# Kernel optimization log

Hardware: AMD Instinct MI355X
Metric: run time of the kernel (lower is better)

The kernel has to match this reference:

```python
import jax, jax.numpy as jnp
import numpy as np

K = 3
EPS = 1e-5

def diff_conv(x, Tf, Tb, W, b):
    terms = [x]
    xf = x
    for _ in range(K):
        xf = jnp.einsum('mn,bnc->bmc', Tf, xf)
        terms.append(xf)
    xb = x
    for _ in range(K):
        xb = jnp.einsum('mn,bnc->bmc', Tb, xb)
        terms.append(xb)
    z = jnp.concatenate(terms, axis=-1)  # (B,N,(2K+1)*C)
    return z @ W + b

def layer_norm(x, gamma, beta):
    mu = jnp.mean(x, axis=-1, keepdims=True)
    var = jnp.var(x, axis=-1, keepdims=True)
    return (x - mu) * jax.lax.rsqrt(var + EPS) * gamma + beta

def dcgru_cell(x, h, Tf, Tb, Wg, bg, Wc, bc, gamma, beta):
    xh = jnp.concatenate([x, h], axis=-1)
    gates = jax.nn.sigmoid(diff_conv(xh, Tf, Tb, Wg, bg))
    r, u = jnp.split(gates, 2, axis=-1)
    xrh = jnp.concatenate([x, r * h], axis=-1)
    c = jnp.tanh(diff_conv(xrh, Tf, Tb, Wc, bc))
    h_new = (1.0 - u) * h + u * c
    return layer_norm(h_new, gamma, beta)

def setup_inputs() -> dict:
    key = jax.random.key(0)
    B, T, N, F, H = 32, 8, 512, 16, 128
    ks = jax.random.split(key, 16)
    s = 0.02
    n_terms = 2 * K + 1
    d0 = (F + H) * n_terms   # layer 0 combined diffusion dim
    d1 = (H + H) * n_terms   # layer 1
    inp = {
        'x_seq': jax.random.normal(ks[0], (B, T, N, F), dtype=jnp.float32),
        'T_f': jax.random.uniform(ks[1], (N, N), dtype=jnp.float32) / N,
        'T_b': jax.random.uniform(ks[2], (N, N), dtype=jnp.float32) / N,
        'Wg0': jax.random.normal(ks[3], (d0, 2 * H), dtype=jnp.float32) * s,
        'bg0': jnp.zeros((2 * H,), dtype=jnp.float32),
        'Wc0': jax.random.normal(ks[4], (d0, H), dtype=jnp.float32) * s,
        'bc0': jnp.zeros((H,), dtype=jnp.float32),
        'g0': jnp.ones((H,), dtype=jnp.float32),
        'be0': jnp.zeros((H,), dtype=jnp.float32),
        'Wg1': jax.random.normal(ks[5], (d1, 2 * H), dtype=jnp.float32) * s,
        'bg1': jnp.zeros((2 * H,), dtype=jnp.float32),
        'Wc1': jax.random.normal(ks[6], (d1, H), dtype=jnp.float32) * s,
        'bc1': jnp.zeros((H,), dtype=jnp.float32),
        'g1': jnp.ones((H,), dtype=jnp.float32),
        'be1': jnp.zeros((H,), dtype=jnp.float32),
    }
    return inp

def reference(x_seq, T_f, T_b, Wg0, bg0, Wc0, bc0, g0, be0, Wg1, bg1, Wc1, bc1, g1, be1):
    B, T, N, F = x_seq.shape
    H = g0.shape[0]
    h0 = jnp.zeros((B, N, H), dtype=x_seq.dtype)
    h1 = jnp.zeros((B, N, H), dtype=x_seq.dtype)

    def step(carry, x_t):
        h0, h1 = carry
        h0 = dcgru_cell(x_t, h0, T_f, T_b, Wg0, bg0, Wc0, bc0, g0, be0)
        h1 = dcgru_cell(h0, h1, T_f, T_b, Wg1, bg1, Wc1, bc1, g1, be1)
        return (h0, h1), None

    xs = jnp.swapaxes(x_seq, 0, 1)  # (T,B,N,F)
    (h0, h1), _ = jax.lax.scan(step, (h0, h1), xs)
    return (h0, h1)
```

## Files before the change

### kernel.cpp

```cpp
#include <hip/hip_runtime.h>
#include <hip/hip_bf16.h>
#include <math.h>

typedef unsigned short u16;
typedef __attribute__((ext_vector_type(8))) short short8;
typedef __attribute__((ext_vector_type(4))) float f32x4;

__device__ __forceinline__ u16 f2bf(float f) {
  union { float f; unsigned u; } v; v.f = f;
  unsigned r = v.u + 0x7fffu + ((v.u >> 16) & 1u);
  return (u16)(r >> 16);
}

__device__ __forceinline__ void glds16(const u16* g, u16* l) {
  __builtin_amdgcn_global_load_lds(
      (const __attribute__((address_space(1))) void*)g,
      (__attribute__((address_space(3))) void*)l, 16, 0, 0);
}

template<int N> __device__ __forceinline__ void kbar() {
  asm volatile("s_waitcnt vmcnt(%0)" :: "n"(N) : "memory");
  __builtin_amdgcn_s_barrier();
  asm volatile("" ::: "memory");
}
__device__ __forceinline__ void bar2() {
  asm volatile("" ::: "memory");
  __builtin_amdgcn_s_barrier();
  asm volatile("" ::: "memory");
}

template<int BM, int BN, int WR, int WC>
__global__ __launch_bounds__(256, 2) void gemm_diff(
    const u16* __restrict__ Tpow, const u16* __restrict__ zT,
    u16* __restrict__ zout, int ldz, int C, int coff0,
    u16* __restrict__ zdual, int Fdual)
{
  constexpr int BK = 64;
  constexpr int FM = BM / (WR * 16), FN = BN / (WC * 16);
  constexpr int SLOTS = (BM + 2 * BN) * 8;
  constexpr int NS = (SLOTS + 255) / 256;
  constexpr int VMIN = SLOTS / 256;
  constexpr int HALF = (BM + 2 * BN) * BK;
  __shared__ u16 sm[2 * HALF];
  const int tid = threadIdx.x, lane = tid & 63, wid = tid >> 6;
  const int wr = wid / WC, wc = wid % WC;
  const int l15 = lane & 15, l4 = lane >> 4;
  const int m0 = blockIdx.x * BM;
  const int y0 = blockIdx.y * BN;
  const int b0 = (blockIdx.z / 6) * 2, tc = blockIdx.z % 6;
  const u16* A = Tpow + (long)tc * 262144;
  const int lb = (tid - lane) * 8;

  const u16* gp[NS];
  #pragma unroll
  for (int i = 0; i < NS; i++) {
    int s = tid + i * 256;
    if (s < BM * 8) {
      int row = s >> 3, kc = s & 7;
      gp[i] = A + (long)(m0 + row) * 512 + (kc ^ (row & 7)) * 8;
    } else {
      int s2 = s - BM * 8;
      int q = s2 / (BN * 8), n = (s2 % (BN * 8)) >> 3, kc = s2 & 7;
      gp[i] = zT + (long)(y0 + n) * 16384 + (b0 + q) * 512 + (kc ^ (n & 7)) * 8;
    }
  }

  auto stage = [&](int buf) {
    u16* base = sm + buf * HALF + lb;
    #pragma unroll
    for (int i = 0; i < NS; i++) {
      if (i * 256 + 256 <= SLOTS || tid < SLOTS - i * 256)
        glds16(gp[i], base + i * 2048);
    }
    #pragma unroll
    for (int i = 0; i < NS; i++) gp[i] += BK;
  };

  f32x4 acc[2][FM][FN] = {};
  auto compute = [&](int buf) {
    const u16* smc = sm + buf * HALF;
    #pragma unroll
    for (int kk = 0; kk < 2; kk++) {
      short8 af[FM], bf[2][FN];
      #pragma unroll
      for (int i = 0; i < FM; i++) {
        int ar = wr * FM * 16 + i * 16 + l15;
        af[i] = *(const short8*)&smc[ar * BK + (((kk * 4 + l4) ^ (ar & 7)) << 3)];
      }
      #pragma unroll
      for (int q = 0; q < 2; q++)
        #pragma unroll
        for (int j = 0; j < FN; j++) {
          int br = wc * FN * 16 + j * 16 + l15;
          bf[q][j] = *(const short8*)&smc[BM * BK + q * BN * BK + br * BK +
                                          (((kk * 4 + l4) ^ (br & 7)) << 3)];
        }
      #pragma unroll
      for (int q = 0; q < 2; q++)
        #pragma unroll
        for (int i = 0; i < FM; i++)
          #pragma unroll
          for (int j = 0; j < FN; j++)
            acc[q][i][j] = __builtin_amdgcn_mfma_f32_16x16x32_bf16(af[i], bf[q][j], acc[q][i][j], 0, 0, 0);
    }
  };

  stage(0);
  int cur = 0;
  for (int t = 0; t < 7; t++) {
    stage(cur ^ 1);
    kbar<VMIN>();
    compute(cur);
    bar2();
    cur ^= 1;
  }
  kbar<0>();
  compute(cur);

  const int tC = (1 + tc) * C;
  #pragma unroll
  for (int q = 0; q < 2; q++) {
    #pragma unroll
    for (int i = 0; i < FM; i++) {
      #pragma unroll
      for (int j = 0; j < FN; j++) {
        int node = m0 + wr * FM * 16 + i * 16 + l4 * 4;
        int ch = y0 + wc * FN * 16 + j * 16 + l15;
        #pragma unroll
        for (int rr = 0; rr < 4; rr++) {
          u16 v = f2bf(acc[q][i][j][rr]);
          long r = (long)(b0 + q) * 512 + node + rr;
          zout[r * ldz + tC + coff0 + ch] = v;
          if (Fdual && ch < Fdual) zdual[r * ldz + tC + ch] = v;
        }
      }
    }
  }
}

template<int BM, int BN>
__global__ __launch_bounds__(256) void gemm_proj(
    const u16* __restrict__ Az, int ldA,
    const u16* __restrict__ W, int K,
    const float* __restrict__ bias,
    const float* __restrict__ hst,
    u16* __restrict__ zc, int ldzc, int Foff,
    u16* __restrict__ zTc,
    float* __restrict__ outbuf)
{
  constexpr int BK = 64;
  constexpr int FM = BM / 32, FN = BN / 32;
  constexpr int NSA = BM / 32, NSB = BN / 32;
  constexpr int VMIN = NSA + NSB;
  constexpr int HALF = (BM + BN) * BK;
  __shared__ u16 sm[2 * HALF];
  const int tid = threadIdx.x, lane = tid & 63, wid = tid >> 6;
  const int wr = wid >> 1, wc = wid & 1;
  const int l15 = lane & 15, l4 = lane >> 4;
  const int m0 = blockIdx.x * BM;
  const int n0 = blockIdx.y * BN;
  const int lb = (tid - lane) * 8;

  const u16* ap[NSA];
  const u16* wp[NSB];
  #pragma unroll
  for (int i = 0; i < NSA; i++) {
    int s = tid + i * 256;
    int row = s >> 3, kc = s & 7;
    int kcg = kc ^ (row & 7);
    ap[i] = Az + (long)(m0 + row) * ldA + kcg * 8;
  }
  #pragma unroll
  for (int i = 0; i < NSB; i++) {
    int s = tid + (NSA + i) * 256;
    int row = s >> 3, kc = s & 7;
    int kcg = kc ^ (row & 7);
    wp[i] = W + (long)(n0 + row - BM) * K + kcg * 8;
  }

  auto stage = [&](int buf) {
    u16* base = sm + buf * HALF + lb;
    #pragma unroll
    for (int i = 0; i < NSA; i++) { glds16(ap[i], base + i * 2048); ap[i] += BK; }
    #pragma unroll
    for (int i = 0; i < NSB; i++) { glds16(wp[i], base + (NSA + i) * 2048); wp[i] += BK; }
  };

  f32x4 acc[FM][FN] = {};
  auto compute = [&](int buf) {
    const u16* smc = sm + buf * HALF;
    #pragma unroll
    for (int kk = 0; kk < 2; kk++) {
      short8 af[FM], bf[FN];
      #pragma unroll
      for (int i = 0; i < FM; i++) {
        int ar = wr * FM * 16 + i * 16 + l15;
        af[i] = *(const short8*)&smc[ar * BK + (((kk * 4 + l4) ^ (ar & 7)) << 3)];
      }
      #pragma unroll
      for (int j = 0; j < FN; j++) {
        int br = wc * FN * 16 + j * 16 + l15;
        bf[j] = *(const short8*)&smc[BM * BK + br * BK + (((kk * 4 + l4) ^ (br & 7)) << 3)];
      }
      #pragma unroll
      for (int i = 0; i < FM; i++)
        #pragma unroll
        for (int j = 0; j < FN; j++)
          acc[i][j] = __builtin_amdgcn_mfma_f32_16x16x32_bf16(af[i], bf[j], acc[i][j], 0, 0, 0);
    }
  };

  stage(0);
  int cur = 0;
  const int NT = K >> 6;
  for (int t = 1; t < NT; t++) {
    stage(cur ^ 1);
    kbar<VMIN>();
    compute(cur);
    bar2();
    cur ^= 1;
  }
  kbar<0>();
  compute(cur);

  #pragma unroll
  for (int i = 0; i < FM; i++) {
    #pragma unroll
    for (int j = 0; j < FN; j++) {
      int mb = m0 + wr * FM * 16 + i * 16 + l4 * 4;
      int n = n0 + wc * FN * 16 + j * 16 + l15;
      #pragma unroll
      for (int rr = 0; rr < 4; rr++) {
        float v = acc[i][j][rr] + bias[n];
        long r = mb + rr;
        float g = 1.f / (1.f + expf(-v));
        if (n < 128) {
          float rh = g * hst[r * 128 + n];
          u16 hv = f2bf(rh);
          zc[r * ldzc + Foff + n] = hv;
          zTc[(long)n * 16384 + r] = hv;
        } else {
          outbuf[r * 128 + (n - 128)] = g;
        }
      }
    }
  }
}

__global__ __launch_bounds__(256) void proj_cand_gru(
    const u16* __restrict__ Ag, const u16* __restrict__ Ac, int ldA,
    const u16* __restrict__ W, int K,
    const float* __restrict__ bias,
    const float* __restrict__ ub, float* __restrict__ h,
    const float* __restrict__ gamma, const float* __restrict__ beta,
    u16* __restrict__ rm0, int ld0, int co0,
    u16* __restrict__ rm1, int ld1, int co1,
    u16* __restrict__ cm0, int ro0,
    u16* __restrict__ cm1, int ro1,
    const float* __restrict__ xs, int tnext,
    u16* __restrict__ xz0g, u16* __restrict__ xz0c, u16* __restrict__ xz0T)
{
  constexpr int BM = 32, BN = 128, BK = 64;
  constexpr int FM = 2, FN = 2;
  constexpr int NSA = 1, NSB = 4;
  constexpr int HALF = (BM + BN) * BK;
  __shared__ u16 sm[2 * HALF];
  const int tid = threadIdx.x, lane = tid & 63, wid = tid >> 6;
  const int wc = wid;
  const int l15 = lane & 15, l4 = lane >> 4;
  const int m0 = blockIdx.x * BM;
  const int lb = (tid - lane) * 8;

  unsigned aoff[NSA];
  const u16* wp[NSB];
  #pragma unroll
  for (int i = 0; i < NSA; i++) {
    int s = tid + i * 256;
    int row = s >> 3, kc = s & 7;
    int kcg = kc ^ (row & 7);
    aoff[i] = (unsigned)((m0 + row) * ldA + kcg * 8);
  }
  #pragma unroll
  for (int i = 0; i < NSB; i++) {
    int s = tid + (NSA + i) * 256;
    int row = (s >> 3) - BM, kc = s & 7;
    int kcg = kc ^ ((row + BM) & 7);
    wp[i] = W + (long)row * K + kcg * 8;
  }

  auto stage = [&](int buf, int koff) {
    u16* base = sm + buf * HALF + lb;
    const u16* ab = ((koff >> 7) & 1) ? Ac : Ag;
    #pragma unroll
    for (int i = 0; i < NSA; i++) glds16(ab + aoff[i] + koff, base + i * 2048);
    #pragma unroll
    for (int i = 0; i < NSB; i++) { glds16(wp[i], base + (NSA + i) * 2048); wp[i] += BK; }
  };

  f32x4 acc[FM][FN] = {};
  auto compute = [&](int buf) {
    const u16* smc = sm + buf * HALF;
    #pragma unroll
    for (int kk = 0; kk < 2; kk++) {
      short8 af[FM], bf[FN];
      #pragma unroll
      for (int i = 0; i < FM; i++) {
        int ar = i * 16 + l15;
        af[i] = *(const short8*)&smc[ar * BK + (((kk * 4 + l4) ^ (ar & 7)) << 3)];
      }
      #pragma unroll
      for (int j = 0; j < FN; j++) {
        int br = wc * 32 + j * 16 + l15;
        bf[j] = *(const short8*)&smc[BM * BK + br * BK + (((kk * 4 + l4) ^ (br & 7)) << 3)];
      }
      #pragma unroll
      for (int i = 0; i < FM; i++)
        #pragma unroll
        for (int j = 0; j < FN; j++)
          acc[i][j] = __builtin_amdgcn_mfma_f32_16x16x32_bf16(af[i], bf[j], acc[i][j], 0, 0, 0);
    }
  };

  stage(0, 0);
  int cur = 0;
  const int NT = K >> 6;
  for (int t = 1; t < NT; t++) {
    stage(cur ^ 1, t * 64);
    kbar<5>();
    compute(cur);
    bar2();
    cur ^= 1;
  }
  kbar<0>();
  compute(cur);
  __syncthreads();

  float* hs = (float*)sm;
  #pragma unroll
  for (int i = 0; i < FM; i++) {
    #pragma unroll
    for (int j = 0; j < FN; j++) {
      #pragma unroll
      for (int rr = 0; rr < 4; rr++) {
        int lrow = i * 16 + l4 * 4 + rr;
        int n = wc * 32 + j * 16 + l15;
        long r = m0 + lrow;
        float c = tanhf(acc[i][j][rr] + bias[n]);
        float u = ub[r * 128 + n];
        float hold = h[r * 128 + n];
        hs[lrow * 132 + n] = (1.f - u) * hold + u * c;
      }
    }
  }
  __syncthreads();

  {
    int row = tid >> 3, g = tid & 7;
    float s = 0.f, s2 = 0.f;
    #pragma unroll
    for (int k = 0; k < 16; k++) {
      float v = hs[row * 132 + g + 8 * k];
      s += v; s2 += v * v;
    }
    s += __shfl_xor(s, 1); s2 += __shfl_xor(s2, 1);
    s += __shfl_xor(s, 2); s2 += __shfl_xor(s2, 2);
    s += __shfl_xor(s, 4); s2 += __shfl_xor(s2, 4);
    float mu = s * (1.f / 128.f);
    float var = s2 * (1.f / 128.f) - mu * mu;
    float rs = rsqrtf(var + 1e-5f);
    long rb = (long)(m0 + row) * 128;
    #pragma unroll
    for (int k = 0; k < 16; k++) {
      int c = g + 8 * k;
      float v = (hs[row * 132 + c] - mu) * rs * gamma[c] + beta[c];
      h[rb + c] = v;
      hs[row * 132 + c] = v;
    }
  }
  __syncthreads();

  #pragma unroll
  for (int i = 0; i < 16; i++) {
    int idx = tid + i * 256;
    int row = idx >> 7, c = idx & 127;
    u16 v = f2bf(hs[row * 132 + c]);
    long r = m0 + row;
    rm0[r * ld0 + co0 + c] = v;
    if (rm1) rm1[r * ld1 + co1 + c] = v;
  }
  {
    const int c2 = tid >> 1, half = tid & 1;
    u16 tmp[16];
    #pragma unroll
    for (int i = 0; i < 16; i++) tmp[i] = f2bf(hs[(half * 16 + i) * 132 + c2]);
    const short8* tv = (const short8*)tmp;
    long off = (long)(ro0 + c2) * 16384 + m0 + half * 16;
    *(short8*)&cm0[off] = tv[0];
    *(short8*)&cm0[off + 8] = tv[1];
    if (cm1) {
      long o2 = (long)(ro1 + c2) * 16384 + m0 + half * 16;
      *(short8*)&cm1[o2] = tv[0];
      *(short8*)&cm1[o2 + 8] = tv[1];
    }
  }
  if (xs) {
    for (int e = tid; e < 512; e += 256) {
      int lrow = e >> 4, f = e & 15;
      long r = m0 + lrow;
      int b = (int)(r >> 9), n = (int)(r & 511);
      u16 v = f2bf(xs[(((long)b * 8 + tnext) * 512 + n) * 16 + f]);
      xz0g[r * 1024 + f] = v;
      xz0c[r * 1024 + f] = v;
      xz0T[(long)f * 16384 + r] = v;
    }
  }
}

__global__ __launch_bounds__(256) void xk(
    const float* __restrict__ xs, int t,
    u16* __restrict__ z0g, u16* __restrict__ z0c, u16* __restrict__ z0Tg)
{
  int r = blockIdx.x * 256 + threadIdx.x;
  int b = r >> 9, n = r & 511;
  const float* src = xs + (((long)b * 8 + t) * 512 + n) * 16;
  u16 tmp[16];
  #pragma unroll
  for (int f = 0; f < 16; f++) tmp[f] = f2bf(src[f]);
  const short8* tv = (const short8*)tmp;
  *(short8*)&z0g[(long)r * 1024] = tv[0];
  *(short8*)&z0g[(long)r * 1024 + 8] = tv[1];
  *(short8*)&z0c[(long)r * 1024] = tv[0];
  *(short8*)&z0c[(long)r * 1024 + 8] = tv[1];
  #pragma unroll
  for (int f = 0; f < 16; f++) z0Tg[(long)f * 16384 + r] = tmp[f];
}

__global__ void cvtT(const float* __restrict__ Tf, const float* __restrict__ Tb,
                     u16* __restrict__ Tpow, u16* __restrict__ TfT, u16* __restrict__ TbT)
{
  int idx = blockIdx.x * 256 + threadIdx.x;
  int i = idx >> 9, j = idx & 511;
  const float* s = blockIdx.y ? Tb : Tf;
  u16* d = Tpow + (blockIdx.y ? 3 : 0) * 262144;
  u16* dT = blockIdx.y ? TbT : TfT;
  u16 v = f2bf(s[idx]);
  d[idx] = v;
  dT[(long)j * 512 + i] = v;
}

__global__ __launch_bounds__(256) void gemm_pow(
    const u16* __restrict__ A0, const u16* __restrict__ B0, u16* __restrict__ C0,
    const u16* __restrict__ A1, const u16* __restrict__ B1, u16* __restrict__ C1)
{
  constexpr int BM = 64, BN = 64, BK = 32;
  __shared__ u16 sm[(BM + BN) * BK];
  const int tid = threadIdx.x, lane = tid & 63, wid = tid >> 6;
  const int wr = wid >> 1, wc = wid & 1;
  const int l15 = lane & 15, l4 = lane >> 4;
  const int m0 = blockIdx.x * BM, n0 = blockIdx.y * BN;
  const u16* A = blockIdx.z ? A1 : A0;
  const u16* Bt = blockIdx.z ? B1 : B0;
  u16* Cc = blockIdx.z ? C1 : C0;

  f32x4 acc[2][2] = {};
  for (int k0 = 0; k0 < 512; k0 += BK) {
    for (int s = tid; s < (BM + BN) * 4; s += 256) {
      const u16* gp;
      if (s < BM * 4) { int m = s >> 2, kc = s & 3; gp = A + (long)(m0 + m) * 512 + k0 + kc * 8; }
      else { int q = s - BM * 4; int n = q >> 2, kc = q & 3; gp = Bt + (long)(n0 + n) * 512 + k0 + kc * 8; }
      glds16(gp, sm + (s - lane) * 8);
    }
    __syncthreads();
    short8 af[2], bf[2];
    #pragma unroll
    for (int i = 0; i < 2; i++)
      af[i] = *(const short8*)&sm[(wr * 32 + i * 16 + l15) * BK + l4 * 8];
    #pragma unroll
    for (int j = 0; j < 2; j++)
      bf[j] = *(const short8*)&sm[BM * BK + (wc * 32 + j * 16 + l15) * BK + l4 * 8];
    #pragma unroll
    for (int i = 0; i < 2; i++)
      #pragma unroll
      for (int j = 0; j < 2; j++)
        acc[i][j] = __builtin_amdgcn_mfma_f32_16x16x32_bf16(af[i], bf[j], acc[i][j], 0, 0, 0);
    __syncthreads();
  }
  #pragma unroll
  for (int i = 0; i < 2; i++)
    #pragma unroll
    for (int j = 0; j < 2; j++) {
      int mb = m0 + wr * 32 + i * 16 + l4 * 4;
      int n = n0 + wc * 32 + j * 16 + l15;
      #pragma unroll
      for (int rr = 0; rr < 4; rr++)
        Cc[(long)(mb + rr) * 512 + n] = f2bf(acc[i][j][rr]);
    }
}

__global__ void wt_cvt(const float* __restrict__ W, u16* __restrict__ Wt,
                       int Ksrc, int Kpad, int Nout) {
  long idx = (long)blockIdx.x * 256 + threadIdx.x;
  if (idx >= (long)Nout * Kpad) return;
  int o = (int)(idx / Kpad), k = (int)(idx % Kpad);
  Wt[idx] = f2bf(k < Ksrc ? W[(long)k * Nout + o] : 0.f);
}

extern "C" void kernel_launch(void* const* d_in, const int* in_sizes, int n_in,
                              void* d_out, int out_size, void* d_ws, size_t ws_size,
                              hipStream_t stream) {
  const float* x_seq = (const float*)d_in[0];
  const float* Tf  = (const float*)d_in[1];
  const float* Tb  = (const float*)d_in[2];
  const float* Wg0 = (const float*)d_in[3];
  const float* bg0 = (const float*)d_in[4];
  const float* Wc0 = (const float*)d_in[5];
  const float* bc0 = (const float*)d_in[6];
  const float* g0  = (const float*)d_in[7];
  const float* be0 = (const float*)d_in[8];
  const float* Wg1 = (const float*)d_in[9];
  const float* bg1 = (const float*)d_in[10];
  const float* Wc1 = (const float*)d_in[11];
  const float* bc1 = (const float*)d_in[12];
  const float* g1  = (const float*)d_in[13];
  const float* be1 = (const float*)d_in[14];

  constexpr int B = 32, T = 8;
  constexpr long M = 16384;

  char* p = (char*)d_ws;
  auto carve = [&](size_t bytes) { char* r = p; p += (bytes + 255) & ~(size_t)255; return r; };
  u16* z0g  = (u16*)carve(M * 1024 * 2);
  u16* z0c  = (u16*)carve(M * 1024 * 2);
  u16* z1g  = (u16*)carve(M * 1792 * 2);
  u16* z1c  = (u16*)carve(M * 1792 * 2);
  u16* z0Tg = (u16*)carve(144L * M * 2);
  u16* z0Tc = (u16*)carve(128L * M * 2);
  u16* z1Tg = (u16*)carve(256L * M * 2);
  u16* z1Tc = (u16*)carve(128L * M * 2);
  float* ubuf = (float*)carve(M * 128 * 4);
  u16* Tpow = (u16*)carve(6L * 512 * 512 * 2);
  u16* TfT  = (u16*)carve(512L * 512 * 2);
  u16* TbT  = (u16*)carve(512L * 512 * 2);
  u16* Wg0t = (u16*)carve(256L * 1024 * 2);
  u16* Wc0t = (u16*)carve(128L * 1024 * 2);
  u16* Wg1t = (u16*)carve(256L * 1792 * 2);
  u16* Wc1t = (u16*)carve(128L * 1792 * 2);

  float* h0 = (float*)d_out;
  float* h1 = h0 + M * 128;

  hipMemsetAsync(d_out, 0, (size_t)out_size * 4, stream);
  hipMemsetAsync(z0g, 0, (size_t)((char*)(z1c + M * 1792) - (char*)z0g), stream);
  hipMemsetAsync(z0Tg + 16L * M, 0, 128L * M * 2, stream);
  hipMemsetAsync(z1Tg + 128L * M, 0, 128L * M * 2, stream);

  cvtT<<<dim3(1024, 2), 256, 0, stream>>>(Tf, Tb, Tpow, TfT, TbT);
  gemm_pow<<<dim3(8, 8, 2), 256, 0, stream>>>(
      Tpow, TfT, Tpow + 1L * 262144, Tpow + 3L * 262144, TbT, Tpow + 4L * 262144);
  gemm_pow<<<dim3(8, 8, 2), 256, 0, stream>>>(
      Tpow + 1L * 262144, TfT, Tpow + 2L * 262144, Tpow + 4L * 262144, TbT, Tpow + 5L * 262144);
  wt_cvt<<<(256 * 1024 + 255) / 256, 256, 0, stream>>>(Wg0, Wg0t, 1008, 1024, 256);
  wt_cvt<<<(128 * 1024 + 255) / 256, 256, 0, stream>>>(Wc0, Wc0t, 1008, 1024, 128);
  wt_cvt<<<(256 * 1792 + 255) / 256, 256, 0, stream>>>(Wg1, Wg1t, 1792, 1792, 256);
  wt_cvt<<<(128 * 1792 + 255) / 256, 256, 0, stream>>>(Wc1, Wc1t, 1792, 1792, 128);

  xk<<<64, 256, 0, stream>>>(x_seq, 0, z0g, z0c, z0Tg);

  for (int t = 0; t < T; t++) {
    if (t == 0) {
      gemm_diff<128, 16, 4, 1><<<dim3(4, 1, 96), 256, 0, stream>>>(
          Tpow, z0Tg, z0g, 1024, 144, 0, z0c, 16);
    } else {
      gemm_diff<128, 48, 4, 1><<<dim3(4, 3, 96), 256, 0, stream>>>(
          Tpow, z0Tg, z0g, 1024, 144, 0, z0c, 16);
    }
    gemm_proj<64, 64><<<dim3(256, 4), 256, 0, stream>>>(
        z0g, 1024, Wg0t, 1024, bg0, h0, z0c, 1024, 16, z0Tc, ubuf);
    if (t > 0)
      gemm_diff<128, 64, 2, 2><<<dim3(4, 2, 96), 256, 0, stream>>>(
          Tpow, z0Tc, z0c, 1024, 144, 16, nullptr, 0);
    proj_cand_gru<<<512, 256, 0, stream>>>(
        z0c, z0c, 1024, Wc0t, 1024, bc0, ubuf, h0, g0, be0,
        z0g, 1024, 16, z1g, 1792, 0, z0Tg, 16, z1Tg, 0,
        nullptr, 0, nullptr, nullptr, nullptr);
    gemm_diff<128, 64, 2, 2><<<dim3(4, (t == 0) ? 2 : 4, 96), 256, 0, stream>>>(
        Tpow, z1Tg, z1g, 1792, 256, 0, nullptr, 0);
    gemm_proj<64, 64><<<dim3(256, 4), 256, 0, stream>>>(
        z1g, 1792, Wg1t, 1792, bg1, h1, z1c, 1792, 128, z1Tc, ubuf);
    if (t > 0)
      gemm_diff<128, 64, 2, 2><<<dim3(4, 2, 96), 256, 0, stream>>>(
          Tpow, z1Tc, z1c, 1792, 256, 128, nullptr, 0);
    proj_cand_gru<<<512, 256, 0, stream>>>(
        z1g, z1c, 1792, Wc1t, 1792, bc1, ubuf, h1, g1, be1,
        z1g, 1792, 128, nullptr, 0, 0, z1Tg, 128, nullptr, 0,
        (t < T - 1) ? x_seq : nullptr, t + 1, z0g, z0c, z0Tg);
  }
}
```

Before: 1.486 ms.

## Wavefront-skew the two DCGRU layers and merge their per-step kernels into joint launches

Reschedules the time loop so that layer 1 at step t runs alongside layer 0 at step t+1. The gate-diffusion, gate-projection and candidate-diffusion GEMMs of both layers are fused into single launches that pick a sub-problem from the block index. This halves the number of dependent kernel launches and fills the GPU better for the small per-layer grids. In exchange it needs a separate u buffer per layer, a prologue and epilogue, and careful ordering of writes to the shared z buffers between layers.

```diff
diff --git a/kernel.cpp b/kernel.cpp
--- a/kernel.cpp
+++ b/kernel.cpp
@@ -30,7 +30,8 @@
 }
 
 template<int BM, int BN, int WR, int WC>
-__global__ __launch_bounds__(256, 2) void gemm_diff(
+__device__ __forceinline__ void diff_body(
+    u16* sm, int bx, int by, int bz,
     const u16* __restrict__ Tpow, const u16* __restrict__ zT,
     u16* __restrict__ zout, int ldz, int C, int coff0,
     u16* __restrict__ zdual, int Fdual)
@@ -41,13 +42,12 @@
   constexpr int NS = (SLOTS + 255) / 256;
   constexpr int VMIN = SLOTS / 256;
   constexpr int HALF = (BM + 2 * BN) * BK;
-  __shared__ u16 sm[2 * HALF];
   const int tid = threadIdx.x, lane = tid & 63, wid = tid >> 6;
   const int wr = wid / WC, wc = wid % WC;
   const int l15 = lane & 15, l4 = lane >> 4;
-  const int m0 = blockIdx.x * BM;
-  const int y0 = blockIdx.y * BN;
-  const int b0 = (blockIdx.z / 6) * 2, tc = blockIdx.z % 6;
+  const int m0 = bx * BM;
+  const int y0 = by * BN;
+  const int b0 = (bz / 6) * 2, tc = bz % 6;
   const u16* A = Tpow + (long)tc * 262144;
   const int lb = (tid - lane) * 8;
 
@@ -138,27 +138,74 @@
   }
 }
 
+template<int BM, int BN, int WR, int WC>
+__global__ __launch_bounds__(256, 2) void gemm_diff(
+    const u16* __restrict__ Tpow, const u16* __restrict__ zT,
+    u16* __restrict__ zout, int ldz, int C, int coff0,
+    u16* __restrict__ zdual, int Fdual)
+{
+  __shared__ u16 sm[2 * (BM + 2 * BN) * 64];
+  diff_body<BM, BN, WR, WC>(sm, blockIdx.x, blockIdx.y, blockIdx.z,
+                            Tpow, zT, zout, ldz, C, coff0, zdual, Fdual);
+}
+
+__global__ __launch_bounds__(256, 2) void gdiff2(
+    const u16* __restrict__ Tpow,
+    const u16* __restrict__ zT1, u16* __restrict__ z1out, int y1sh, int r1cnt,
+    const u16* __restrict__ zT0, u16* __restrict__ z0out, u16* __restrict__ z0dual)
+{
+  __shared__ u16 sm[2 * (128 + 2 * 64) * 64];
+  int b = blockIdx.x;
+  if (b < r1cnt) {
+    int bx = b & 3, rem = b >> 2;
+    int by = rem & ((1 << y1sh) - 1), bz = rem >> y1sh;
+    diff_body<128, 64, 2, 2>(sm, bx, by, bz, Tpow, zT1, z1out, 1792, 256, 0, nullptr, 0);
+  } else {
+    int b2 = b - r1cnt;
+    int bx = b2 & 3, rem = b2 >> 2;
+    int by = rem % 3, bz = rem / 3;
+    diff_body<128, 48, 4, 1>(sm, bx, by, bz, Tpow, zT0, z0out, 1024, 144, 0, z0dual, 16);
+  }
+}
+
+__global__ __launch_bounds__(256, 2) void cdiff2(
+    const u16* __restrict__ Tpow,
+    const u16* __restrict__ zTc1, u16* __restrict__ z1c, int r1cnt,
+    const u16* __restrict__ zTc0, u16* __restrict__ z0c)
+{
+  __shared__ u16 sm[2 * (128 + 2 * 64) * 64];
+  int b = blockIdx.x;
+  if (b < r1cnt) {
+    int bx = b & 3, rem = b >> 2;
+    int by = rem & 1, bz = rem >> 1;
+    diff_body<128, 64, 2, 2>(sm, bx, by, bz, Tpow, zTc1, z1c, 1792, 256, 128, nullptr, 0);
+  } else {
+    int b2 = b - r1cnt;
+    int bx = b2 & 3, rem = b2 >> 2;
+    int by = rem & 1, bz = rem >> 1;
+    diff_body<128, 64, 2, 2>(sm, bx, by, bz, Tpow, zTc0, z0c, 1024, 144, 16, nullptr, 0);
+  }
+}
+
 template<int BM, int BN>
-__global__ __launch_bounds__(256) void gemm_proj(
+__device__ __forceinline__ void proj_body(
+    u16* sm, int mb, int nb,
     const u16* __restrict__ Az, int ldA,
     const u16* __restrict__ W, int K,
-    const float* __restrict__ bias,
-    const float* __restrict__ hst,
+    const float* __restrict__ bias, const float* __restrict__ hst,
     u16* __restrict__ zc, int ldzc, int Foff,
-    u16* __restrict__ zTc,
-    float* __restrict__ outbuf)
+    u16* __restrict__ zTc, float* __restrict__ outbuf)
 {
   constexpr int BK = 64;
   constexpr int FM = BM / 32, FN = BN / 32;
   constexpr int NSA = BM / 32, NSB = BN / 32;
   constexpr int VMIN = NSA + NSB;
   constexpr int HALF = (BM + BN) * BK;
-  __shared__ u16 sm[2 * HALF];
   const int tid = threadIdx.x, lane = tid & 63, wid = tid >> 6;
   const int wr = wid >> 1, wc = wid & 1;
   const int l15 = lane & 15, l4 = lane >> 4;
-  const int m0 = blockIdx.x * BM;
-  const int n0 = blockIdx.y * BN;
+  const int m0 = mb * BM;
+  const int n0 = nb * BN;
   const int lb = (tid - lane) * 8;
 
   const u16* ap[NSA];
@@ -167,15 +214,13 @@
   for (int i = 0; i < NSA; i++) {
     int s = tid + i * 256;
     int row = s >> 3, kc = s & 7;
-    int kcg = kc ^ (row & 7);
-    ap[i] = Az + (long)(m0 + row) * ldA + kcg * 8;
+    ap[i] = Az + (long)(m0 + row) * ldA + (kc ^ (row & 7)) * 8;
   }
   #pragma unroll
   for (int i = 0; i < NSB; i++) {
     int s = tid + (NSA + i) * 256;
     int row = s >> 3, kc = s & 7;
-    int kcg = kc ^ (row & 7);
-    wp[i] = W + (long)(n0 + row - BM) * K + kcg * 8;
+    wp[i] = W + (long)(n0 + row - BM) * K + (kc ^ (row & 7)) * 8;
   }
 
   auto stage = [&](int buf) {
@@ -227,12 +272,12 @@
   for (int i = 0; i < FM; i++) {
     #pragma unroll
     for (int j = 0; j < FN; j++) {
-      int mb = m0 + wr * FM * 16 + i * 16 + l4 * 4;
+      int mbv = m0 + wr * FM * 16 + i * 16 + l4 * 4;
       int n = n0 + wc * FN * 16 + j * 16 + l15;
       #pragma unroll
       for (int rr = 0; rr < 4; rr++) {
         float v = acc[i][j][rr] + bias[n];
-        long r = mb + rr;
+        long r = mbv + rr;
         float g = 1.f / (1.f + expf(-v));
         if (n < 128) {
           float rh = g * hst[r * 128 + n];
@@ -244,6 +289,24 @@
         }
       }
     }
+  }
+}
+
+__global__ __launch_bounds__(256) void gproj2(
+    const u16* __restrict__ A1, int ldA1, const u16* __restrict__ W1, int K1,
+    const float* __restrict__ b1, const float* __restrict__ h1s,
+    u16* __restrict__ zc1, int Foff1, u16* __restrict__ zT1c, float* __restrict__ ub1,
+    const u16* __restrict__ A0, const u16* __restrict__ W0,
+    const float* __restrict__ b0, const float* __restrict__ h0s,
+    u16* __restrict__ zc0, u16* __restrict__ zT0c, float* __restrict__ ub0)
+{
+  __shared__ u16 sm[2 * (64 + 64) * 64];
+  int b = blockIdx.x;
+  if (b < 1024) {
+    proj_body<64, 64>(sm, b & 255, b >> 8, A1, ldA1, W1, K1, b1, h1s, zc1, ldA1, Foff1, zT1c, ub1);
+  } else {
+    int b2 = b - 1024;
+    proj_body<64, 64>(sm, b2 & 255, b2 >> 8, A0, 1024, W0, 1024, b0, h0s, zc0, 1024, 16, zT0c, ub0);
   }
 }
 
@@ -277,15 +340,13 @@
   for (int i = 0; i < NSA; i++) {
     int s = tid + i * 256;
     int row = s >> 3, kc = s & 7;
-    int kcg = kc ^ (row & 7);
-    aoff[i] = (unsigned)((m0 + row) * ldA + kcg * 8);
+    aoff[i] = (unsigned)((m0 + row) * ldA + (kc ^ (row & 7)) * 8);
   }
   #pragma unroll
   for (int i = 0; i < NSB; i++) {
     int s = tid + (NSA + i) * 256;
     int row = (s >> 3) - BM, kc = s & 7;
-    int kcg = kc ^ ((row + BM) & 7);
-    wp[i] = W + (long)row * K + kcg * 8;
+    wp[i] = W + (long)row * K + (kc ^ ((row + BM) & 7)) * 8;
   }
 
   auto stage = [&](int buf, int koff) {
@@ -524,7 +585,6 @@
   const float* g1  = (const float*)d_in[13];
   const float* be1 = (const float*)d_in[14];
 
-  constexpr int B = 32, T = 8;
   constexpr long M = 16384;
 
   char* p = (char*)d_ws;
@@ -537,7 +597,8 @@
   u16* z0Tc = (u16*)carve(128L * M * 2);
   u16* z1Tg = (u16*)carve(256L * M * 2);
   u16* z1Tc = (u16*)carve(128L * M * 2);
-  float* ubuf = (float*)carve(M * 128 * 4);
+  float* ubuf0 = (float*)carve(M * 128 * 4);
+  float* ubuf1 = (float*)carve(M * 128 * 4);
   u16* Tpow = (u16*)carve(6L * 512 * 512 * 2);
   u16* TfT  = (u16*)carve(512L * 512 * 2);
   u16* TbT  = (u16*)carve(512L * 512 * 2);
@@ -565,34 +626,44 @@
   wt_cvt<<<(128 * 1792 + 255) / 256, 256, 0, stream>>>(Wc1, Wc1t, 1792, 1792, 128);
 
   xk<<<64, 256, 0, stream>>>(x_seq, 0, z0g, z0c, z0Tg);
-
-  for (int t = 0; t < T; t++) {
-    if (t == 0) {
-      gemm_diff<128, 16, 4, 1><<<dim3(4, 1, 96), 256, 0, stream>>>(
-          Tpow, z0Tg, z0g, 1024, 144, 0, z0c, 16);
-    } else {
-      gemm_diff<128, 48, 4, 1><<<dim3(4, 3, 96), 256, 0, stream>>>(
-          Tpow, z0Tg, z0g, 1024, 144, 0, z0c, 16);
-    }
-    gemm_proj<64, 64><<<dim3(256, 4), 256, 0, stream>>>(
-        z0g, 1024, Wg0t, 1024, bg0, h0, z0c, 1024, 16, z0Tc, ubuf);
-    if (t > 0)
-      gemm_diff<128, 64, 2, 2><<<dim3(4, 2, 96), 256, 0, stream>>>(
-          Tpow, z0Tc, z0c, 1024, 144, 16, nullptr, 0);
+  gemm_diff<128, 16, 4, 1><<<dim3(4, 1, 96), 256, 0, stream>>>(
+      Tpow, z0Tg, z0g, 1024, 144, 0, z0c, 16);
+  gproj2<<<1024, 256, 0, stream>>>(
+      z0g, 1024, Wg0t, 1024, bg0, h0, z0c, 16, z0Tc, ubuf0,
+      z0g, Wc0t, bc0, h0, z0c, z0Tc, ubuf0);
+  proj_cand_gru<<<512, 256, 0, stream>>>(
+      z0c, z0c, 1024, Wc0t, 1024, bc0, ubuf0, h0, g0, be0,
+      z0g, 1024, 16, z1g, 1792, 0, z0Tg, 16, z1Tg, 0,
+      x_seq, 1, z0g, z0c, z0Tg);
+
+  for (int tt = 0; tt < 7; tt++) {
+    int y1sh = (tt == 0) ? 1 : 2;
+    int r1 = 4 * (1 << y1sh) * 96;
+    gdiff2<<<r1 + 1152, 256, 0, stream>>>(
+        Tpow, z1Tg, z1g, y1sh, r1, z0Tg, z0g, z0c);
+    gproj2<<<2048, 256, 0, stream>>>(
+        z1g, 1792, Wg1t, 1792, bg1, h1, z1c, 128, z1Tc, ubuf1,
+        z0g, Wg0t, bg0, h0, z0c, z0Tc, ubuf0);
+    int c1 = (tt == 0) ? 0 : 768;
+    cdiff2<<<c1 + 768, 256, 0, stream>>>(
+        Tpow, z1Tc, z1c, c1, z0Tc, z0c);
     proj_cand_gru<<<512, 256, 0, stream>>>(
-        z0c, z0c, 1024, Wc0t, 1024, bc0, ubuf, h0, g0, be0,
+        z1g, z1c, 1792, Wc1t, 1792, bc1, ubuf1, h1, g1, be1,
+        z1g, 1792, 128, nullptr, 0, 0, z1Tg, 128, nullptr, 0,
+        nullptr, 0, nullptr, nullptr, nullptr);
+    proj_cand_gru<<<512, 256, 0, stream>>>(
+        z0c, z0c, 1024, Wc0t, 1024, bc0, ubuf0, h0, g0, be0,
         z0g, 1024, 16, z1g, 1792, 0, z0Tg, 16, z1Tg, 0,
-        nullptr, 0, nullptr, nullptr, nullptr);
-    gemm_diff<128, 64, 2, 2><<<dim3(4, (t == 0) ? 2 : 4, 96), 256, 0, stream>>>(
-        Tpow, z1Tg, z1g, 1792, 256, 0, nullptr, 0);
-    gemm_proj<64, 64><<<dim3(256, 4), 256, 0, stream>>>(
-        z1g, 1792, Wg1t, 1792, bg1, h1, z1c, 1792, 128, z1Tc, ubuf);
-    if (t > 0)
-      gemm_diff<128, 64, 2, 2><<<dim3(4, 2, 96), 256, 0, stream>>>(
-          Tpow, z1Tc, z1c, 1792, 256, 128, nullptr, 0);
-    proj_cand_gru<<<512, 256, 0, stream>>>(
-        z1g, z1c, 1792, Wc1t, 1792, bc1, ubuf, h1, g1, be1,
-        z1g, 1792, 128, nullptr, 0, 0, z1Tg, 128, nullptr, 0,
-        (t < T - 1) ? x_seq : nullptr, t + 1, z0g, z0c, z0Tg);
-  }
-}
+        (tt + 2 <= 7) ? x_seq : nullptr, tt + 2, z0g, z0c, z0Tg);
+  }
+
+  gdiff2<<<1536, 256, 0, stream>>>(Tpow, z1Tg, z1g, 2, 1536, z0Tg, z0g, z0c);
+  gproj2<<<1024, 256, 0, stream>>>(
+      z1g, 1792, Wg1t, 1792, bg1, h1, z1c, 128, z1Tc, ubuf1,
+      z0g, Wg0t, bg0, h0, z0c, z0Tc, ubuf0);
+  cdiff2<<<768, 256, 0, stream>>>(Tpow, z1Tc, z1c, 768, z0Tc, z0c);
+  proj_cand_gru<<<512, 256, 0, stream>>>(
+      z1g, z1c, 1792, Wc1t, 1792, bc1, ubuf1, h1, g1, be1,
+      z1g, 1792, 128, nullptr, 0, 0, z1Tg, 128, nullptr, 0,
+      nullptr, 0, nullptr, nullptr, nullptr);
+}
```

Result: faster. 1.397 ms (-6.0%).
